# Performance work log

Measured on AMD Instinct MI355X. Metric: run time of the kernel, lower is better.

## Reference

```python
import jax, jax.numpy as jnp
import numpy as np

B, T, D = 8, 4096, 1024


def setup_inputs() -> dict:
    key = jax.random.key(0)
    ks = jax.random.split(key, 7)
    s = 1.0 / np.sqrt(D)
    return {
        "x": jax.random.normal(ks[0], (B, T, D), dtype=jnp.float32),
        "Wi": jax.random.uniform(ks[1], (D, D), jnp.float32, -s, s),
        "bi": jax.random.uniform(ks[2], (D,), jnp.float32, -s, s),
        "Wg": jax.random.uniform(ks[3], (D, D), jnp.float32, -s, s),
        "bg": jax.random.uniform(ks[4], (D,), jnp.float32, -s, s),
        "Wo": jax.random.uniform(ks[5], (D, D), jnp.float32, -s, s),
        "bo": jax.random.uniform(ks[6], (D,), jnp.float32, -s, s),
    }


def _rg_lru(x, Wi, bi, Wg, bg, Wo, bo):
    # Projections (torch Linear: x @ W.T + b)
    u = jnp.einsum("btd,ed->bte", x, Wi) + bi          # [B,T,D]
    g = jax.nn.sigmoid(jnp.einsum("btd,ed->bte", x, Wg) + bg)

    # Gated linear recurrence: h_t = g_t * h_{t-1} + (1 - g_t) * u_t
    def step(h, gu):
        g_t, u_t = gu
        h = g_t * h + (1.0 - g_t) * u_t
        return h, h

    h0 = jnp.zeros((x.shape[0], x.shape[2]), dtype=u.dtype)
    # scan over time: move T to leading axis
    _, h = jax.lax.scan(step, h0, (jnp.swapaxes(g, 0, 1), jnp.swapaxes(u, 0, 1)))
    h = jnp.swapaxes(h, 0, 1)                           # [B,T,D]
    return jnp.einsum("btd,ed->bte", h, Wo) + bo


def reference(x, Wi, bi, Wg, bg, Wo, bo):
    return _rg_lru(x, Wi, bi, Wg, bg, Wo, bo)
```

## Files before the change

kernel.cpp:

```cpp
#include <hip/hip_runtime.h>
#include <hip/hip_bf16.h>

#define B_  8
#define T_  4096
#define D_  1024
#define M_  (B_*T_)

#define BM 128
#define BN 128
#define BK 32

#define TC      64
#define NCHUNK  (T_/TC)

typedef short bf16x8 __attribute__((ext_vector_type(8)));
typedef float f32x4  __attribute__((ext_vector_type(4)));

__device__ __forceinline__ unsigned short f2bfu(float f) {
  __hip_bfloat16 b = __float2bfloat16(f);
  unsigned short s; __builtin_memcpy(&s, &b, 2); return s;
}
__device__ __forceinline__ float bfu2f(unsigned short v) {
  unsigned int t = ((unsigned int)v) << 16;
  float f; __builtin_memcpy(&f, &t, 4); return f;
}

__global__ __launch_bounds__(256) void cast_f32_bf16(const float* __restrict__ in,
                                                     unsigned short* __restrict__ out,
                                                     long long n) {
  size_t i = ((size_t)blockIdx.x * 256 + threadIdx.x) * 4;
  if (i >= (size_t)n) return;
  float4 v = *reinterpret_cast<const float4*>(in + i);
  ushort4 o = make_ushort4(f2bfu(v.x), f2bfu(v.y), f2bfu(v.z), f2bfu(v.w));
  *reinterpret_cast<ushort4*>(out + i) = o;
}

template<int EPI>
__global__ __launch_bounds__(256) void gemm_bt(
    const __hip_bfloat16* __restrict__ A,
    const __hip_bfloat16* __restrict__ Bt,
    const float* __restrict__ bias,
    void* __restrict__ Cout, int M, int N, int K)
{
  __shared__ __align__(16) __hip_bfloat16 As[BM*BK];
  __shared__ __align__(16) __hip_bfloat16 Bs[BN*BK];

  const int tid = threadIdx.x;
  const int w   = tid >> 6;
  const int l   = tid & 63;
  const int wr  = (w >> 1) * 64;
  const int wc  = (w & 1)  * 64;
  const int lr  = l & 15;
  const int lk  = (l >> 4) * 8;

  const int brow = blockIdx.x * BM;
  const int bcol = blockIdx.y * BN;

  const int srow = w*32 + (l >> 2);
  const int sk   = (l & 3) * 8;

  const __hip_bfloat16* Ag = A  + (size_t)(brow + srow)*K + sk;
  const __hip_bfloat16* Bg = Bt + (size_t)(bcol + srow)*K + sk;

  char* AsB = (char*)As + w*2048;
  char* BsB = (char*)Bs + w*2048;

  f32x4 acc[4][4] = {};

  for (int k0 = 0; k0 < K; k0 += BK) {
    __syncthreads();
#pragma unroll
    for (int j = 0; j < 2; ++j) {
      __builtin_amdgcn_global_load_lds(
          (const __attribute__((address_space(1))) void*)(Ag + (size_t)j*16*K + k0),
          (__attribute__((address_space(3))) void*)(AsB + j*1024), 16, 0, 0);
      __builtin_amdgcn_global_load_lds(
          (const __attribute__((address_space(1))) void*)(Bg + (size_t)j*16*K + k0),
          (__attribute__((address_space(3))) void*)(BsB + j*1024), 16, 0, 0);
    }
    __syncthreads();

    bf16x8 af[4], bfr[4];
#pragma unroll
    for (int m = 0; m < 4; ++m)
      af[m] = *reinterpret_cast<const bf16x8*>(As + (wr + m*16 + lr)*BK + lk);
#pragma unroll
    for (int n = 0; n < 4; ++n)
      bfr[n] = *reinterpret_cast<const bf16x8*>(Bs + (wc + n*16 + lr)*BK + lk);
#pragma unroll
    for (int m = 0; m < 4; ++m)
#pragma unroll
      for (int n = 0; n < 4; ++n)
        acc[m][n] = __builtin_amdgcn_mfma_f32_16x16x32_bf16(af[m], bfr[n], acc[m][n], 0, 0, 0);
  }

  float bv[4];
#pragma unroll
  for (int n = 0; n < 4; ++n) bv[n] = bias[bcol + wc + n*16 + lr];

#pragma unroll
  for (int m = 0; m < 4; ++m) {
#pragma unroll
    for (int n = 0; n < 4; ++n) {
      const int col = bcol + wc + n*16 + lr;
#pragma unroll
      for (int j = 0; j < 4; ++j) {
        const int row = brow + wr + m*16 + (l >> 4)*4 + j;
        float v = acc[m][n][j] + bv[n];
        if (EPI == 2) v = 1.0f / (1.0f + __expf(-v));
        if (EPI == 0) ((float*)Cout)[(size_t)row*N + col] = v;
        else          ((unsigned short*)Cout)[(size_t)row*N + col] = f2bfu(v);
      }
    }
  }
}

__global__ __launch_bounds__(256) void scan_phase1(
    const __hip_bfloat16* __restrict__ g,
    const __hip_bfloat16* __restrict__ u,
    unsigned short* __restrict__ hloc,
    unsigned short* __restrict__ Aout,
    float* __restrict__ P, float* __restrict__ Hend)
{
  const int d = blockIdx.x * 256 + threadIdx.x;
  const int c = blockIdx.y;
  const int b = blockIdx.z;
  size_t idx = ((size_t)b*T_ + (size_t)c*TC) * D_ + d;
  float h = 0.0f, A = 1.0f;
#pragma unroll 4
  for (int t = 0; t < TC; ++t, idx += D_) {
    float gv = __bfloat162float(g[idx]);
    float uv = __bfloat162float(u[idx]);
    h = gv*h + (1.0f - gv)*uv;
    A *= gv;
    hloc[idx] = f2bfu(h);
    Aout[idx] = f2bfu(A);
  }
  const size_t ci = ((size_t)b*NCHUNK + c)*D_ + d;
  P[ci]    = A;
  Hend[ci] = h;
}

__global__ __launch_bounds__(256) void scan_phase2(
    const float* __restrict__ P, const float* __restrict__ Hend,
    float* __restrict__ carry)
{
  const int gid = blockIdx.x * 256 + threadIdx.x;
  const int b  = gid / D_;
  const int dd = gid % D_;
  float cy = 0.0f;
#pragma unroll 4
  for (int c = 0; c < NCHUNK; ++c) {
    const size_t ci = ((size_t)b*NCHUNK + c)*D_ + dd;
    carry[ci] = cy;
    cy = Hend[ci] + P[ci]*cy;
  }
}

__global__ __launch_bounds__(256) void scan_phase3(
    unsigned short* __restrict__ h,
    const unsigned short* __restrict__ Aout,
    const float* __restrict__ carry)
{
  const size_t i4  = (size_t)blockIdx.x * 256 + threadIdx.x;
  const int d4     = D_ / 4;
  const int dd4    = (int)(i4 % d4);
  const size_t bt  = i4 / d4;
  const int t      = (int)(bt % T_);
  const int b      = (int)(bt / T_);
  const int c      = t / TC;
  const size_t idx = bt * D_ + (size_t)dd4 * 4;

  ushort4 hv = *reinterpret_cast<const ushort4*>(h + idx);
  ushort4 av = *reinterpret_cast<const ushort4*>(Aout + idx);
  float4  cv = *reinterpret_cast<const float4*>(carry + ((size_t)b*NCHUNK + c)*D_ + (size_t)dd4*4);

  ushort4 o;
  o.x = f2bfu(bfu2f(hv.x) + bfu2f(av.x)*cv.x);
  o.y = f2bfu(bfu2f(hv.y) + bfu2f(av.y)*cv.y);
  o.z = f2bfu(bfu2f(hv.z) + bfu2f(av.z)*cv.z);
  o.w = f2bfu(bfu2f(hv.w) + bfu2f(av.w)*cv.w);
  *reinterpret_cast<ushort4*>(h + idx) = o;
}

extern "C" void kernel_launch(void* const* d_in, const int* in_sizes, int n_in,
                              void* d_out, int out_size, void* d_ws, size_t ws_size,
                              hipStream_t stream) {
  const float* x  = (const float*)d_in[0];
  const float* Wi = (const float*)d_in[1];
  const float* bi = (const float*)d_in[2];
  const float* Wg = (const float*)d_in[3];
  const float* bg = (const float*)d_in[4];
  const float* Wo = (const float*)d_in[5];
  const float* bo = (const float*)d_in[6];

  const size_t NX = (size_t)M_ * D_;
  const size_t NW = (size_t)D_ * D_;
  const size_t NC = (size_t)B_ * NCHUNK * D_;

  char* p = (char*)d_ws;
  __hip_bfloat16* xb  = (__hip_bfloat16*)p; p += NX*2;
  __hip_bfloat16* wib = (__hip_bfloat16*)p; p += NW*2;
  __hip_bfloat16* wgb = (__hip_bfloat16*)p; p += NW*2;
  __hip_bfloat16* wob = (__hip_bfloat16*)p; p += NW*2;
  unsigned short* ub  = (unsigned short*)p; p += NX*2;
  unsigned short* gb  = (unsigned short*)p; p += NX*2;
  unsigned short* hb  = (unsigned short*)p; p += NX*2;
  unsigned short* Ab  = (unsigned short*)p; p += NX*2;
  float* P     = (float*)p; p += NC*4;
  float* Hend  = (float*)p; p += NC*4;
  float* carry = (float*)p; p += NC*4;

  cast_f32_bf16<<<(int)(NX/4/256), 256, 0, stream>>>(x,  (unsigned short*)xb,  (long long)NX);
  cast_f32_bf16<<<(int)(NW/4/256), 256, 0, stream>>>(Wi, (unsigned short*)wib, (long long)NW);
  cast_f32_bf16<<<(int)(NW/4/256), 256, 0, stream>>>(Wg, (unsigned short*)wgb, (long long)NW);
  cast_f32_bf16<<<(int)(NW/4/256), 256, 0, stream>>>(Wo, (unsigned short*)wob, (long long)NW);

  dim3 gg(M_/BM, D_/BN);
  gemm_bt<1><<<gg, 256, 0, stream>>>(xb, wib, bi, (void*)ub, M_, D_, D_);
  gemm_bt<2><<<gg, 256, 0, stream>>>(xb, wgb, bg, (void*)gb, M_, D_, D_);

  scan_phase1<<<dim3(D_/256, NCHUNK, B_), 256, 0, stream>>>(
      (const __hip_bfloat16*)gb, (const __hip_bfloat16*)ub, hb, Ab, P, Hend);
  scan_phase2<<<(B_*D_)/256, 256, 0, stream>>>(P, Hend, carry);
  scan_phase3<<<(int)(NX/4/256), 256, 0, stream>>>(hb, Ab, carry);

  gemm_bt<0><<<gg, 256, 0, stream>>>((const __hip_bfloat16*)hb, wob, bo,
                                     d_out, M_, D_, D_);
}
```

Measured before the change: 647.2 us.

## Use 256x256 double-buffered swizzled GEMM and recompute scan instead of storing A

Replaces the 128x128 single-buffered GEMM with a 256x256, 512-thread kernel that uses a 128KB double-buffered LDS, XOR-swizzled layout, split barriers and s_setprio to overlap loads with MFMA. The scan is restructured so phase1 only emits chunk summaries and phase3 re-runs the recurrence from the carry, which drops the hloc/Aout intermediate writes and reads. Scan kernels are also vectorized to four channels per thread. Costs are heavy LDS use (one block per CU) and redundant recurrence arithmetic.

```diff
diff --git a/kernel.cpp b/kernel.cpp
--- a/kernel.cpp
+++ b/kernel.cpp
@@ -5,11 +5,7 @@
 #define T_  4096
 #define D_  1024
 #define M_  (B_*T_)
-
-#define BM 128
-#define BN 128
-#define BK 32
-
+#define NT  16
 #define TC      64
 #define NCHUNK  (T_/TC)
 
@@ -35,110 +31,136 @@
   *reinterpret_cast<ushort4*>(out + i) = o;
 }
 
+
+#define GLL(gsrc, loff) __builtin_amdgcn_global_load_lds( \
+  (const __attribute__((address_space(1))) void*)(gsrc), \
+  (__attribute__((address_space(3))) void*)(lds + (loff)), 16, 0, 0)
+
+#define STAGE(basePtr, matOff, cbuf, kkh, k0g) do { \
+  GLL((basePtr) + (size_t)(k0g) + (kkh)*32, \
+      (cbuf)*65536 + (matOff) + (kkh)*16384 + (w*32)*64); \
+  GLL((basePtr) + (size_t)(k0g) + (kkh)*32 + 16*1024, \
+      (cbuf)*65536 + (matOff) + (kkh)*16384 + (w*32 + 16)*64); \
+} while (0)
+
+#define GATE4 asm volatile("s_waitcnt vmcnt(4)" ::: "memory")
+#define NOGATE (void)0
+
+#define PH(kk, mh, LOADB, STAGE_STMT, GATE_STMT) do { \
+  _Pragma("unroll") \
+  for (int q = 0; q < 4; ++q) \
+    aF[q] = *reinterpret_cast<const bf16x8*>(lds + c*65536 + (kk)*16384 + ((mh)*4+q)*1024 + aoff); \
+  if (LOADB) { \
+    _Pragma("unroll") \
+    for (int q = 0; q < 4; ++q) \
+      bF[q] = *reinterpret_cast<const bf16x8*>(lds + c*65536 + 32768 + (kk)*16384 + q*1024 + boff); \
+  } \
+  STAGE_STMT; \
+  __builtin_amdgcn_s_barrier(); \
+  __builtin_amdgcn_s_setprio(1); \
+  _Pragma("unroll") \
+  for (int q = 0; q < 4; ++q) { \
+    _Pragma("unroll") \
+    for (int n = 0; n < 4; ++n) \
+      acc[(mh)*4+q][n] = __builtin_amdgcn_mfma_f32_16x16x32_bf16(aF[q], bF[n], acc[(mh)*4+q][n], 0, 0, 0); \
+  } \
+  __builtin_amdgcn_s_setprio(0); \
+  GATE_STMT; \
+  __builtin_amdgcn_s_barrier(); \
+} while (0)
+
 template<int EPI>
-__global__ __launch_bounds__(256) void gemm_bt(
+__global__ __launch_bounds__(512, 2) void gemm256(
     const __hip_bfloat16* __restrict__ A,
     const __hip_bfloat16* __restrict__ Bt,
     const float* __restrict__ bias,
-    void* __restrict__ Cout, int M, int N, int K)
-{
-  __shared__ __align__(16) __hip_bfloat16 As[BM*BK];
-  __shared__ __align__(16) __hip_bfloat16 Bs[BN*BK];
+    void* __restrict__ Cout)
+{
+  __shared__ __align__(1024) char lds[131072];
 
   const int tid = threadIdx.x;
-  const int w   = tid >> 6;
-  const int l   = tid & 63;
-  const int wr  = (w >> 1) * 64;
-  const int wc  = (w & 1)  * 64;
-  const int lr  = l & 15;
-  const int lk  = (l >> 4) * 8;
-
-  const int brow = blockIdx.x * BM;
-  const int bcol = blockIdx.y * BN;
-
-  const int srow = w*32 + (l >> 2);
-  const int sk   = (l & 3) * 8;
-
-  const __hip_bfloat16* Ag = A  + (size_t)(brow + srow)*K + sk;
-  const __hip_bfloat16* Bg = Bt + (size_t)(bcol + srow)*K + sk;
-
-  char* AsB = (char*)As + w*2048;
-  char* BsB = (char*)Bs + w*2048;
-
-  f32x4 acc[4][4] = {};
-
-  for (int k0 = 0; k0 < K; k0 += BK) {
-    __syncthreads();
-#pragma unroll
-    for (int j = 0; j < 2; ++j) {
-      __builtin_amdgcn_global_load_lds(
-          (const __attribute__((address_space(1))) void*)(Ag + (size_t)j*16*K + k0),
-          (__attribute__((address_space(3))) void*)(AsB + j*1024), 16, 0, 0);
-      __builtin_amdgcn_global_load_lds(
-          (const __attribute__((address_space(1))) void*)(Bg + (size_t)j*16*K + k0),
-          (__attribute__((address_space(3))) void*)(BsB + j*1024), 16, 0, 0);
-    }
-    __syncthreads();
-
-    bf16x8 af[4], bfr[4];
-#pragma unroll
-    for (int m = 0; m < 4; ++m)
-      af[m] = *reinterpret_cast<const bf16x8*>(As + (wr + m*16 + lr)*BK + lk);
-#pragma unroll
-    for (int n = 0; n < 4; ++n)
-      bfr[n] = *reinterpret_cast<const bf16x8*>(Bs + (wc + n*16 + lr)*BK + lk);
-#pragma unroll
-    for (int m = 0; m < 4; ++m)
-#pragma unroll
-      for (int n = 0; n < 4; ++n)
-        acc[m][n] = __builtin_amdgcn_mfma_f32_16x16x32_bf16(af[m], bfr[n], acc[m][n], 0, 0, 0);
-  }
+  const int w  = tid >> 6;
+  const int l  = tid & 63;
+  const int wm = w >> 2;
+  const int wn = w & 3;
+  const int lr = l & 15;
+  const int hk = l >> 4;
+
+  const int brow = blockIdx.x * 256;
+  const int bcol = blockIdx.y * 256;
+
+  const int srow  = l >> 2;
+  const int sslot = (l & 3) ^ ((l >> 3) & 3);
+  const __hip_bfloat16* Abase = A  + (size_t)(brow + w*32 + srow)*1024 + sslot*8;
+  const __hip_bfloat16* Bbase = Bt + (size_t)(bcol + w*32 + srow)*1024 + sslot*8;
+
+  const int aoff = (wm*128 + lr)*64 + ((hk ^ ((lr >> 1) & 3)) * 16);
+  const int boff = (wn*64  + lr)*64 + ((hk ^ ((lr >> 1) & 3)) * 16);
+
+  f32x4 acc[8][4] = {};
+  bf16x8 aF[4], bF[4];
+
+  STAGE(Abase, 0,     0, 0, 0);
+  STAGE(Bbase, 32768, 0, 0, 0);
+  STAGE(Abase, 0,     0, 1, 0);
+  STAGE(Bbase, 32768, 0, 1, 0);
+  GATE4;
+  __builtin_amdgcn_s_barrier();
+
+  for (int t = 0; t < NT; ++t) {
+    const int c  = t & 1;
+    const int cn = c ^ 1;
+    const int k0n = (t + 1 < NT ? t + 1 : 0) * 64;
+    PH(0, 0, 1, STAGE(Abase, 0,     cn, 0, k0n), NOGATE);
+    PH(0, 1, 0, STAGE(Bbase, 32768, cn, 0, k0n), GATE4);
+    PH(1, 0, 1, STAGE(Abase, 0,     cn, 1, k0n), NOGATE);
+    PH(1, 1, 0, STAGE(Bbase, 32768, cn, 1, k0n), GATE4);
+  }
+  asm volatile("s_waitcnt vmcnt(0)" ::: "memory");
 
   float bv[4];
 #pragma unroll
-  for (int n = 0; n < 4; ++n) bv[n] = bias[bcol + wc + n*16 + lr];
-
-#pragma unroll
-  for (int m = 0; m < 4; ++m) {
+  for (int n = 0; n < 4; ++n) bv[n] = bias[bcol + wn*64 + n*16 + lr];
+
+#pragma unroll
+  for (int mi = 0; mi < 8; ++mi) {
 #pragma unroll
     for (int n = 0; n < 4; ++n) {
-      const int col = bcol + wc + n*16 + lr;
+      const int col = bcol + wn*64 + n*16 + lr;
 #pragma unroll
       for (int j = 0; j < 4; ++j) {
-        const int row = brow + wr + m*16 + (l >> 4)*4 + j;
-        float v = acc[m][n][j] + bv[n];
+        const int row = brow + wm*128 + mi*16 + hk*4 + j;
+        float v = acc[mi][n][j] + bv[n];
         if (EPI == 2) v = 1.0f / (1.0f + __expf(-v));
-        if (EPI == 0) ((float*)Cout)[(size_t)row*N + col] = v;
-        else          ((unsigned short*)Cout)[(size_t)row*N + col] = f2bfu(v);
+        if (EPI == 0) ((float*)Cout)[(size_t)row*D_ + col] = v;
+        else          ((unsigned short*)Cout)[(size_t)row*D_ + col] = f2bfu(v);
       }
     }
   }
 }
 
 __global__ __launch_bounds__(256) void scan_phase1(
-    const __hip_bfloat16* __restrict__ g,
-    const __hip_bfloat16* __restrict__ u,
-    unsigned short* __restrict__ hloc,
-    unsigned short* __restrict__ Aout,
+    const unsigned short* __restrict__ g,
+    const unsigned short* __restrict__ u,
     float* __restrict__ P, float* __restrict__ Hend)
 {
-  const int d = blockIdx.x * 256 + threadIdx.x;
-  const int c = blockIdx.y;
-  const int b = blockIdx.z;
-  size_t idx = ((size_t)b*T_ + (size_t)c*TC) * D_ + d;
-  float h = 0.0f, A = 1.0f;
+  const int c = blockIdx.x, b = blockIdx.y;
+  const int d0 = threadIdx.x * 4;
+  size_t idx = (((size_t)b*T_ + (size_t)c*TC) * D_ + d0) / 4;
+  const ushort4* g4 = reinterpret_cast<const ushort4*>(g);
+  const ushort4* u4 = reinterpret_cast<const ushort4*>(u);
+  float h[4] = {0,0,0,0}, A[4] = {1,1,1,1};
 #pragma unroll 4
-  for (int t = 0; t < TC; ++t, idx += D_) {
-    float gv = __bfloat162float(g[idx]);
-    float uv = __bfloat162float(u[idx]);
-    h = gv*h + (1.0f - gv)*uv;
-    A *= gv;
-    hloc[idx] = f2bfu(h);
-    Aout[idx] = f2bfu(A);
-  }
-  const size_t ci = ((size_t)b*NCHUNK + c)*D_ + d;
-  P[ci]    = A;
-  Hend[ci] = h;
+  for (int t = 0; t < TC; ++t, idx += D_/4) {
+    ushort4 gv = g4[idx], uv = u4[idx];
+    float gf[4] = {bfu2f(gv.x), bfu2f(gv.y), bfu2f(gv.z), bfu2f(gv.w)};
+    float uf[4] = {bfu2f(uv.x), bfu2f(uv.y), bfu2f(uv.z), bfu2f(uv.w)};
+#pragma unroll
+    for (int k = 0; k < 4; ++k) { h[k] = gf[k]*h[k] + (1.0f - gf[k])*uf[k]; A[k] *= gf[k]; }
+  }
+  const size_t ci = ((size_t)b*NCHUNK + c)*D_ + d0;
+  *reinterpret_cast<float4*>(P + ci)    = make_float4(A[0], A[1], A[2], A[3]);
+  *reinterpret_cast<float4*>(Hend + ci) = make_float4(h[0], h[1], h[2], h[3]);
 }
 
 __global__ __launch_bounds__(256) void scan_phase2(
@@ -146,8 +168,8 @@
     float* __restrict__ carry)
 {
   const int gid = blockIdx.x * 256 + threadIdx.x;
-  const int b  = gid / D_;
-  const int dd = gid % D_;
+  const int b  = gid >> 10;
+  const int dd = gid & (D_ - 1);
   float cy = 0.0f;
 #pragma unroll 4
   for (int c = 0; c < NCHUNK; ++c) {
@@ -158,29 +180,30 @@
 }
 
 __global__ __launch_bounds__(256) void scan_phase3(
-    unsigned short* __restrict__ h,
-    const unsigned short* __restrict__ Aout,
-    const float* __restrict__ carry)
-{
-  const size_t i4  = (size_t)blockIdx.x * 256 + threadIdx.x;
-  const int d4     = D_ / 4;
-  const int dd4    = (int)(i4 % d4);
-  const size_t bt  = i4 / d4;
-  const int t      = (int)(bt % T_);
-  const int b      = (int)(bt / T_);
-  const int c      = t / TC;
-  const size_t idx = bt * D_ + (size_t)dd4 * 4;
-
-  ushort4 hv = *reinterpret_cast<const ushort4*>(h + idx);
-  ushort4 av = *reinterpret_cast<const ushort4*>(Aout + idx);
-  float4  cv = *reinterpret_cast<const float4*>(carry + ((size_t)b*NCHUNK + c)*D_ + (size_t)dd4*4);
-
-  ushort4 o;
-  o.x = f2bfu(bfu2f(hv.x) + bfu2f(av.x)*cv.x);
-  o.y = f2bfu(bfu2f(hv.y) + bfu2f(av.y)*cv.y);
-  o.z = f2bfu(bfu2f(hv.z) + bfu2f(av.z)*cv.z);
-  o.w = f2bfu(bfu2f(hv.w) + bfu2f(av.w)*cv.w);
-  *reinterpret_cast<ushort4*>(h + idx) = o;
+    const unsigned short* __restrict__ g,
+    const unsigned short* __restrict__ u,
+    const float* __restrict__ carry,
+    unsigned short* __restrict__ hout)
+{
+  const int c = blockIdx.x, b = blockIdx.y;
+  const int d0 = threadIdx.x * 4;
+  size_t idx = (((size_t)b*T_ + (size_t)c*TC) * D_ + d0) / 4;
+  const ushort4* g4 = reinterpret_cast<const ushort4*>(g);
+  const ushort4* u4 = reinterpret_cast<const ushort4*>(u);
+  ushort4* h4 = reinterpret_cast<ushort4*>(hout);
+  float4 cv = *reinterpret_cast<const float4*>(carry + ((size_t)b*NCHUNK + c)*D_ + d0);
+  float h[4] = {cv.x, cv.y, cv.z, cv.w};
+#pragma unroll 4
+  for (int t = 0; t < TC; ++t, idx += D_/4) {
+    ushort4 gv = g4[idx], uv = u4[idx];
+#pragma unroll
+    for (int k = 0; k < 4; ++k) {
+      float gf = bfu2f(k==0?gv.x:k==1?gv.y:k==2?gv.z:gv.w);
+      float uf = bfu2f(k==0?uv.x:k==1?uv.y:k==2?uv.z:uv.w);
+      h[k] = gf*h[k] + (1.0f - gf)*uf;
+    }
+    h4[idx] = make_ushort4(f2bfu(h[0]), f2bfu(h[1]), f2bfu(h[2]), f2bfu(h[3]));
+  }
 }
 
 extern "C" void kernel_launch(void* const* d_in, const int* in_sizes, int n_in,
@@ -206,7 +229,6 @@
   unsigned short* ub  = (unsigned short*)p; p += NX*2;
   unsigned short* gb  = (unsigned short*)p; p += NX*2;
   unsigned short* hb  = (unsigned short*)p; p += NX*2;
-  unsigned short* Ab  = (unsigned short*)p; p += NX*2;
   float* P     = (float*)p; p += NC*4;
   float* Hend  = (float*)p; p += NC*4;
   float* carry = (float*)p; p += NC*4;
@@ -216,15 +238,13 @@
   cast_f32_bf16<<<(int)(NW/4/256), 256, 0, stream>>>(Wg, (unsigned short*)wgb, (long long)NW);
   cast_f32_bf16<<<(int)(NW/4/256), 256, 0, stream>>>(Wo, (unsigned short*)wob, (long long)NW);
 
-  dim3 gg(M_/BM, D_/BN);
-  gemm_bt<1><<<gg, 256, 0, stream>>>(xb, wib, bi, (void*)ub, M_, D_, D_);
-  gemm_bt<2><<<gg, 256, 0, stream>>>(xb, wgb, bg, (void*)gb, M_, D_, D_);
-
-  scan_phase1<<<dim3(D_/256, NCHUNK, B_), 256, 0, stream>>>(
-      (const __hip_bfloat16*)gb, (const __hip_bfloat16*)ub, hb, Ab, P, Hend);
+  dim3 gg(M_/256, D_/256);
+  gemm256<1><<<gg, 512, 0, stream>>>(xb, wib, bi, (void*)ub);
+  gemm256<2><<<gg, 512, 0, stream>>>(xb, wgb, bg, (void*)gb);
+
+  scan_phase1<<<dim3(NCHUNK, B_), 256, 0, stream>>>(gb, ub, P, Hend);
   scan_phase2<<<(B_*D_)/256, 256, 0, stream>>>(P, Hend, carry);
-  scan_phase3<<<(int)(NX/4/256), 256, 0, stream>>>(hb, Ab, carry);
-
-  gemm_bt<0><<<gg, 256, 0, stream>>>((const __hip_bfloat16*)hb, wob, bo,
-                                     d_out, M_, D_, D_);
-}
+  scan_phase3<<<dim3(NCHUNK, B_), 256, 0, stream>>>(gb, ub, carry, hb);
+
+  gemm256<0><<<gg, 512, 0, stream>>>((const __hip_bfloat16*)hb, wob, bo, d_out);
+}
```

After: 533.1 us. -17.6%, faster.
